# Optimization experiments

Hardware: AMD Instinct MI355X
Metric: run time of the kernel (lower is better)

Reference implementation:

```python
import jax, jax.numpy as jnp
from jax import lax
import numpy as np

B, L, V, E, D, T = 512, 200, 50000, 256, 256, 6
H = D // 2          # per-direction LSTM hidden
SLOPE = 0.01        # LeakyReLU negative slope
START, STOP = 4, 5  # tag_map['START'], tag_map['STOP']


def setup_inputs():
    key = jax.random.key(0)
    ks = jax.random.split(key, 18)
    w = lambda k, shape, scale=0.05: jax.random.normal(k, shape, jnp.float32) * scale
    trans = jax.random.normal(ks[17], (T, T), jnp.float32)
    trans = trans.at[:, START].set(-1000.0)
    trans = trans.at[STOP, :].set(-1000.0)
    return {
        "sentences": jax.random.randint(ks[0], (B, L), 0, V),
        "real_length": jnp.full((B,), L, dtype=jnp.int32),
        "emb": jax.random.normal(ks[1], (V, E), jnp.float32),
        "Wih_f": w(ks[2], (4 * H, E)), "Whh_f": w(ks[3], (4 * H, H)),
        "bih_f": w(ks[4], (4 * H,)),   "bhh_f": w(ks[5], (4 * H,)),
        "Wih_b": w(ks[6], (4 * H, E)), "Whh_b": w(ks[7], (4 * H, H)),
        "bih_b": w(ks[8], (4 * H,)),   "bhh_b": w(ks[9], (4 * H,)),
        "W1": w(ks[10], (D, D)), "b1": w(ks[11], (D,)),
        "W2": w(ks[12], (D, D)), "b2": w(ks[13], (D,)),
        "Wt": w(ks[14], (T, D)), "bt": w(ks[15], (T,)),
        "transitions": trans,
    }


def _leaky(x):
    return jnp.where(x >= 0, x, SLOPE * x)


def _lstm_dir(x, Wih, Whh, bih, bhh):
    # x: [B, L, E] -> hidden states [B, L, H]; PyTorch gate order i,f,g,o
    Bn = x.shape[0]
    Hn = Whh.shape[1]
    xg = jnp.einsum('ble,ge->blg', x, Wih) + bih + bhh  # [B, L, 4H]
    def step(carry, xt):
        h, c = carry
        g = xt + h @ Whh.T
        i, f, gg, o = jnp.split(g, 4, axis=-1)
        c = jax.nn.sigmoid(f) * c + jax.nn.sigmoid(i) * jnp.tanh(gg)
        h = jax.nn.sigmoid(o) * jnp.tanh(c)
        return (h, c), h
    init = (jnp.zeros((Bn, Hn), x.dtype), jnp.zeros((Bn, Hn), x.dtype))
    _, hs = lax.scan(step, init, jnp.swapaxes(xg, 0, 1))  # [L, B, H]
    return jnp.swapaxes(hs, 0, 1)


def _emissions(sentences, emb, Wih_f, Whh_f, bih_f, bhh_f, Wih_b, Whh_b, bih_b, bhh_b,
               W1, b1, W2, b2, Wt, bt):
    x = emb[sentences]                                   # [B, L, E]
    hf = _lstm_dir(x, Wih_f, Whh_f, bih_f, bhh_f)
    hb = _lstm_dir(x[:, ::-1], Wih_b, Whh_b, bih_b, bhh_b)[:, ::-1]
    h = jnp.concatenate([hf, hb], axis=-1)               # [B, L, D]
    h = _leaky(h @ W1.T + b1)
    h = _leaky(h @ W2.T + b2)
    return _leaky(h @ Wt.T + bt)                         # [B, L, T]


def _viterbi(logits, transitions):
    # logits: [L, T]; trellis recursion then backtrace
    def step(prev, obs):
        v = prev[:, None] + transitions                  # [T, T]
        tr = obs + jnp.max(v, axis=0)
        return tr, jnp.argmax(v, axis=0)
    last, bps = lax.scan(step, logits[0], logits[1:])    # bps: [L-1, T]
    score = jnp.max(last)
    last_tag = jnp.argmax(last)
    def back(tag, bp):
        new = bp[tag]
        return new, new
    _, prevs = lax.scan(back, last_tag, bps[::-1])
    path = jnp.concatenate([prevs[::-1], last_tag[None]])  # [L]
    return score, path


def reference(sentences, real_length, emb, Wih_f, Whh_f, bih_f, bhh_f,
              Wih_b, Whh_b, bih_b, bhh_b, W1, b1, W2, b2, Wt, bt, transitions):
    # real_length is full (=L) for every sample, so pack/pad is the identity,
    # matching the original forward's lengths=[i.size(-1)] behavior.
    logits = _emissions(sentences, emb, Wih_f, Whh_f, bih_f, bhh_f,
                        Wih_b, Whh_b, bih_b, bhh_b, W1, b1, W2, b2, Wt, bt)
    scores, paths = jax.vmap(_viterbi, in_axes=(0, None))(logits, transitions)
    return scores, paths
```

## Files before the change

### kernel.cpp

```cpp
#include <hip/hip_runtime.h>
#include <cmath>

#define B_   512
#define L_   200
#define V_   50000
#define E_   256
#define H_   128
#define G4H_ 512
#define D_   256
#define T_   6

__device__ __forceinline__ float sigmoidf_(float x) { return 1.0f / (1.0f + __expf(-x)); }
__device__ __forceinline__ float leakyf_(float x)   { return x >= 0.0f ? x : 0.01f * x; }

template<int CTRL>
__device__ __forceinline__ float dpp_add_(float x) {
    const int m = __builtin_amdgcn_mov_dpp(__float_as_int(x), CTRL, 0xF, 0xF, true);
    return x + __int_as_float(m);
}

#define XBM 128
#define XBN 128
#define XBK 8
#define XSTR 132

__global__ __launch_bounds__(256) void gemm_xg_chunk(
    const int* __restrict__ sent, const float* __restrict__ emb,
    const float* __restrict__ Wf, const float* __restrict__ Wb,
    const float* __restrict__ bihf, const float* __restrict__ bhhf,
    const float* __restrict__ bihb, const float* __restrict__ bhhb,
    float* __restrict__ xgc, int c0, int tc)
{
    __shared__ float As[2][XBK][XSTR];
    __shared__ float Bs[2][XBK][XSTR];
    __shared__ int   tok[XBM];

    const int bm  = blockIdx.x;
    const int bn  = blockIdx.y;
    const int tid = threadIdx.x;
    const int half = B_ * tc;
    const int dir  = (bm * XBM) >= half;

    if (tid < XBM) {
        const int vm  = bm * XBM + tid;
        const int rem = vm - dir * half;
        const int b   = rem / tc;
        const int ti  = rem - b * tc;
        const int s   = c0 + ti;
        const int t   = dir ? (L_ - 1 - s) : s;
        tok[tid] = sent[b * L_ + t];
    }
    __syncthreads();

    const int tx = tid & 15;
    const int ty = tid >> 4;
    const int n0 = bn * XBN;

    const float* W   = dir ? Wb   : Wf;
    const float* bih = dir ? bihb : bihf;
    const float* bhh = dir ? bhhb : bhhf;

    const int am = tid >> 1;
    const int ak = (tid & 1) * 4;

    const float* arow = emb + (size_t)tok[am] * E_ + ak;
    const float* brow = W + (size_t)(n0 + am) * E_ + ak;

    float acc[8][8];
#pragma unroll
    for (int i = 0; i < 8; ++i)
#pragma unroll
        for (int j = 0; j < 8; ++j) acc[i][j] = 0.0f;

    {
        const float4 a = *(const float4*)(arow);
        const float4 b = *(const float4*)(brow);
        As[0][ak + 0][am] = a.x; As[0][ak + 1][am] = a.y;
        As[0][ak + 2][am] = a.z; As[0][ak + 3][am] = a.w;
        Bs[0][ak + 0][am] = b.x; Bs[0][ak + 1][am] = b.y;
        Bs[0][ak + 2][am] = b.z; Bs[0][ak + 3][am] = b.w;
    }
    __syncthreads();

    const int NIT = E_ / XBK;
    for (int it = 0; it < NIT; ++it) {
        const int cur = it & 1;
        const int kn  = (it + 1) * XBK;
        float4 na, nb;
        if (kn < E_) {
            na = *(const float4*)(arow + kn);
            nb = *(const float4*)(brow + kn);
        }
#pragma unroll
        for (int k = 0; k < XBK; ++k) {
            float a[8], bb[8];
            *(float4*)a        = *(const float4*)&As[cur][k][ty * 4];
            *(float4*)(a + 4)  = *(const float4*)&As[cur][k][64 + ty * 4];
            *(float4*)(bb)     = *(const float4*)&Bs[cur][k][tx * 4];
            *(float4*)(bb + 4) = *(const float4*)&Bs[cur][k][64 + tx * 4];
#pragma unroll
            for (int i = 0; i < 8; ++i)
#pragma unroll
                for (int j = 0; j < 8; ++j) acc[i][j] += a[i] * bb[j];
        }
        if (kn < E_) {
            const int nxt = cur ^ 1;
            As[nxt][ak + 0][am] = na.x; As[nxt][ak + 1][am] = na.y;
            As[nxt][ak + 2][am] = na.z; As[nxt][ak + 3][am] = na.w;
            Bs[nxt][ak + 0][am] = nb.x; Bs[nxt][ak + 1][am] = nb.y;
            Bs[nxt][ak + 2][am] = nb.z; Bs[nxt][ak + 3][am] = nb.w;
        }
        __syncthreads();
    }

    const int nb0i = n0 + tx * 4;
    const int nb1i = n0 + 64 + tx * 4;
    float bias[8];
#pragma unroll
    for (int j = 0; j < 4; ++j) {
        bias[j]     = bih[nb0i + j] + bhh[nb0i + j];
        bias[4 + j] = bih[nb1i + j] + bhh[nb1i + j];
    }
#pragma unroll
    for (int i = 0; i < 8; ++i) {
        const int row = bm * XBM + ((i < 4) ? (ty * 4 + i) : (64 + ty * 4 + i - 4));
        float* dst = xgc + (size_t)row * G4H_;
        float4 v0, v1;
        v0.x = acc[i][0] + bias[0]; v0.y = acc[i][1] + bias[1];
        v0.z = acc[i][2] + bias[2]; v0.w = acc[i][3] + bias[3];
        v1.x = acc[i][4] + bias[4]; v1.y = acc[i][5] + bias[5];
        v1.z = acc[i][6] + bias[6]; v1.w = acc[i][7] + bias[7];
        *(float4*)(dst + nb0i) = v0;
        *(float4*)(dst + nb1i) = v1;
    }
}

__global__ __launch_bounds__(512, 2) void lstm_scan_chunk(
    const float* __restrict__ xgc,
    const float* __restrict__ Whh_f, const float* __restrict__ Whh_b,
    float* __restrict__ state, float* __restrict__ hcat, int c0, int tc)
{
    const int wg  = blockIdx.x;
    const int dir = wg >> 7;
    const int b0  = (wg & 127) * 4;
    const int tid = threadIdx.x;

    const int q  = tid & 3;
    const int g2 = tid >> 2;
    const int j_ = g2;
    const int s_ = q;

    const float* Whh = dir ? Whh_b : Whh_f;

    float w[4][32];
#pragma unroll
    for (int p = 0; p < 4; ++p) {
        const float* wr = Whh + (size_t)(g2 + 128 * p) * H_ + q * 32;
#pragma unroll
        for (int kk = 0; kk < 32; kk += 4) {
            const float4 v = *(const float4*)(wr + kk);
            w[p][kk] = v.x; w[p][kk + 1] = v.y; w[p][kk + 2] = v.z; w[p][kk + 3] = v.w;
        }
    }

    __shared__ float hbuf[4 * 132];
    __shared__ float gbuf[4 * 528];

    float c;
    if (c0 == 0) {
        hbuf[(j_ >> 5) * 132 + (j_ & 31) * 4 + s_] = 0.0f;
        c = 0.0f;
    } else {
        hbuf[(j_ >> 5) * 132 + (j_ & 31) * 4 + s_] =
            state[((size_t)(dir * B_ + b0 + s_) * 2 + 0) * H_ + j_];
        c = state[((size_t)(dir * B_ + b0 + s_) * 2 + 1) * H_ + j_];
    }

    const int t0    = dir ? (L_ - 1 - c0) : c0;
    const int hstep = dir ? -D_ : D_;
    const int grow  = g2 + 128 * q;

    const float* xp[4];
#pragma unroll
    for (int s = 0; s < 4; ++s)
        xp[s] = xgc + ((size_t)(dir * B_ + b0 + s) * tc) * G4H_ + grow;
    float* hp = hcat + ((size_t)(b0 + s_) * L_ + t0) * D_ + dir * H_ + j_;

    const float* hq = hbuf + q * 132;

    __syncthreads();

    for (int t = 0; t < tc; ++t) {
        float xv[4];
#pragma unroll
        for (int s = 0; s < 4; ++s) { xv[s] = xp[s][0]; xp[s] += G4H_; }

        float acc[4][4];
#pragma unroll
        for (int p = 0; p < 4; ++p)
#pragma unroll
            for (int s = 0; s < 4; ++s) acc[p][s] = 0.0f;

#pragma unroll
        for (int kk = 0; kk < 32; ++kk) {
            const float4 hv = *(const float4*)(hq + kk * 4);
#pragma unroll
            for (int p = 0; p < 4; ++p) {
                acc[p][0] += w[p][kk] * hv.x;
                acc[p][1] += w[p][kk] * hv.y;
                acc[p][2] += w[p][kk] * hv.z;
                acc[p][3] += w[p][kk] * hv.w;
            }
        }

#pragma unroll
        for (int p = 0; p < 4; ++p)
#pragma unroll
            for (int s = 0; s < 4; ++s) {
                float v = acc[p][s];
                v = dpp_add_<0xB1>(v);
                v = dpp_add_<0x4E>(v);
                acc[p][s] = v;
            }

        float o0 = acc[0][0], o1 = acc[0][1], o2 = acc[0][2], o3 = acc[0][3];
        if (q == 1) { o0 = acc[1][0]; o1 = acc[1][1]; o2 = acc[1][2]; o3 = acc[1][3]; }
        if (q == 2) { o0 = acc[2][0]; o1 = acc[2][1]; o2 = acc[2][2]; o3 = acc[2][3]; }
        if (q == 3) { o0 = acc[3][0]; o1 = acc[3][1]; o2 = acc[3][2]; o3 = acc[3][3]; }
        *(float4*)(gbuf + q * 528 + g2 * 4) =
            make_float4(o0 + xv[0], o1 + xv[1], o2 + xv[2], o3 + xv[3]);
        __syncthreads();

        {
            const float gi = gbuf[0 * 528 + j_ * 4 + s_];
            const float gf = gbuf[1 * 528 + j_ * 4 + s_];
            const float gg = gbuf[2 * 528 + j_ * 4 + s_];
            const float go = gbuf[3 * 528 + j_ * 4 + s_];
            c = sigmoidf_(gf) * c + sigmoidf_(gi) * tanhf(gg);
            const float hv = sigmoidf_(go) * tanhf(c);
            hbuf[(j_ >> 5) * 132 + (j_ & 31) * 4 + s_] = hv;
            hp[0] = hv;
            hp += hstep;
        }
        __syncthreads();
    }

    state[((size_t)(dir * B_ + b0 + s_) * 2 + 0) * H_ + j_] =
        hbuf[(j_ >> 5) * 132 + (j_ & 31) * 4 + s_];
    state[((size_t)(dir * B_ + b0 + s_) * 2 + 1) * H_ + j_] = c;
}

#define BM 64
#define BN 128
#define BK 16
#define ASTR 68
#define BSTR 132
#define S1T 68

__global__ __launch_bounds__(256) void fused_mlp(
    const float* __restrict__ hcat,
    const float* __restrict__ W1, const float* __restrict__ b1,
    const float* __restrict__ W2, const float* __restrict__ b2,
    const float* __restrict__ Wt, const float* __restrict__ bt,
    float* __restrict__ logits)
{
    __shared__ float As[BK][ASTR];
    __shared__ float Bs[BK][BSTR];
    __shared__ float h1T[BN][S1T];
    __shared__ float Wt_s[T_][D_ + 2];
    __shared__ float b1_s[D_], b2_s[D_], bt_s[T_];

    const int tid  = threadIdx.x;
    const int row0 = blockIdx.x * BM;

    for (int i = tid; i < T_ * D_; i += 256) Wt_s[i >> 8][i & 255] = Wt[i];
    b1_s[tid] = b1[tid];
    b2_s[tid] = b2[tid];
    if (tid < T_) bt_s[tid] = bt[tid];

    const int tx = tid & 15;
    const int ty = tid >> 4;
    const int lrow = tid >> 2;
    const int lk   = (tid & 3) * 4;

    const float* arow = hcat + (size_t)(row0 + lrow) * D_ + lk;

    float acc2[2][4][8];
#pragma unroll
    for (int q = 0; q < 2; ++q)
#pragma unroll
        for (int i = 0; i < 4; ++i)
#pragma unroll
            for (int j = 0; j < 8; ++j) acc2[q][i][j] = 0.0f;

    for (int n0t = 0; n0t < 2; ++n0t) {
        const int n0 = n0t * BN;

        float acc1[4][8];
#pragma unroll
        for (int i = 0; i < 4; ++i)
#pragma unroll
            for (int j = 0; j < 8; ++j) acc1[i][j] = 0.0f;

        for (int k0 = 0; k0 < D_; k0 += BK) {
            {
                const float4 v = *(const float4*)(arow + k0);
                As[lk + 0][lrow] = v.x; As[lk + 1][lrow] = v.y;
                As[lk + 2][lrow] = v.z; As[lk + 3][lrow] = v.w;
            }
#pragma unroll
            for (int p = 0; p < 2; ++p) {
                const int n = p * 64 + lrow;
                const float4 v = *(const float4*)(W1 + (size_t)(n0 + n) * D_ + k0 + lk);
                Bs[lk + 0][n] = v.x; Bs[lk + 1][n] = v.y;
                Bs[lk + 2][n] = v.z; Bs[lk + 3][n] = v.w;
            }
            __syncthreads();
#pragma unroll
            for (int k = 0; k < BK; ++k) {
                float a[4], bb[8];
                *(float4*)a        = *(const float4*)&As[k][ty * 4];
                *(float4*)(bb)     = *(const float4*)&Bs[k][tx * 4];
                *(float4*)(bb + 4) = *(const float4*)&Bs[k][64 + tx * 4];
#pragma unroll
                for (int i = 0; i < 4; ++i)
#pragma unroll
                    for (int j = 0; j < 8; ++j) acc1[i][j] += a[i] * bb[j];
            }
            __syncthreads();
        }

#pragma unroll
        for (int j = 0; j < 8; ++j) {
            const int nl = (j < 4) ? (tx * 4 + j) : (64 + tx * 4 + j - 4);
            const float bv = b1_s[n0 + nl];
            float4 v;
            v.x = leakyf_(acc1[0][j] + bv);
            v.y = leakyf_(acc1[1][j] + bv);
            v.z = leakyf_(acc1[2][j] + bv);
            v.w = leakyf_(acc1[3][j] + bv);
            *(float4*)&h1T[nl][ty * 4] = v;
        }
        __syncthreads();

#pragma unroll
        for (int n2t = 0; n2t < 2; ++n2t) {
            for (int kc = 0; kc < BN; kc += BK) {
#pragma unroll
                for (int p = 0; p < 2; ++p) {
                    const int n = p * 64 + lrow;
                    const float4 v = *(const float4*)(W2 + (size_t)(n2t * BN + n) * D_ + n0 + kc + lk);
                    Bs[lk + 0][n] = v.x; Bs[lk + 1][n] = v.y;
                    Bs[lk + 2][n] = v.z; Bs[lk + 3][n] = v.w;
                }
                __syncthreads();
#pragma unroll
                for (int k = 0; k < BK; ++k) {
                    float a[4], bb[8];
                    *(float4*)a        = *(const float4*)&h1T[kc + k][ty * 4];
                    *(float4*)(bb)     = *(const float4*)&Bs[k][tx * 4];
                    *(float4*)(bb + 4) = *(const float4*)&Bs[k][64 + tx * 4];
#pragma unroll
                    for (int i = 0; i < 4; ++i)
#pragma unroll
                        for (int j = 0; j < 8; ++j) acc2[n2t][i][j] += a[i] * bb[j];
                }
                __syncthreads();
            }
        }
    }

    float part[4][T_];
#pragma unroll
    for (int i = 0; i < 4; ++i)
#pragma unroll
        for (int jt = 0; jt < T_; ++jt) part[i][jt] = 0.0f;

#pragma unroll
    for (int q = 0; q < 2; ++q)
#pragma unroll
        for (int j = 0; j < 8; ++j) {
            const int n = q * BN + ((j < 4) ? (tx * 4 + j) : (64 + tx * 4 + j - 4));
            const float bv = b2_s[n];
            float h2v[4];
#pragma unroll
            for (int i = 0; i < 4; ++i) h2v[i] = leakyf_(acc2[q][i][j] + bv);
#pragma unroll
            for (int jt = 0; jt < T_; ++jt) {
                const float wv = Wt_s[jt][n];
#pragma unroll
                for (int i = 0; i < 4; ++i) part[i][jt] += h2v[i] * wv;
            }
        }

#pragma unroll
    for (int m = 1; m <= 8; m <<= 1)
#pragma unroll
        for (int i = 0; i < 4; ++i)
#pragma unroll
            for (int jt = 0; jt < T_; ++jt)
                part[i][jt] += __shfl_xor(part[i][jt], m, 16);

    if (tx == 0) {
#pragma unroll
        for (int i = 0; i < 4; ++i) {
            const int m = row0 + ty * 4 + i;
#pragma unroll
            for (int jt = 0; jt < T_; ++jt)
                logits[(size_t)m * T_ + jt] = leakyf_(part[i][jt] + bt_s[jt]);
        }
    }
}

__global__ __launch_bounds__(64) void viterbi_kernel(
    const float* __restrict__ logits, const float* __restrict__ trans,
    float* __restrict__ out)
{
    const int b = blockIdx.x;
    const int lane = threadIdx.x;

    __shared__ unsigned char bp[L_][8];
    __shared__ int path_s[L_];

    float tr[T_];
    if (lane < T_) {
#pragma unroll
        for (int i = 0; i < T_; ++i) tr[i] = trans[i * T_ + lane];
    }
    const float* lg = logits + (size_t)b * L_ * T_;
    float prev = (lane < T_) ? lg[lane] : -1e30f;

    for (int t = 1; t < L_; ++t) {
        float m = -1e30f; int arg = 0;
#pragma unroll
        for (int i = 0; i < T_; ++i) {
            const float v = __shfl(prev, i, 64) + tr[i];
            if (v > m) { m = v; arg = i; }
        }
        const float obs = (lane < T_) ? lg[t * T_ + lane] : 0.0f;
        prev = obs + m;
        if (lane < T_) bp[t][lane] = (unsigned char)arg;
    }
    __syncthreads();

    float best = __shfl(prev, 0, 64); int tag = 0;
#pragma unroll
    for (int jj = 1; jj < T_; ++jj) {
        const float v = __shfl(prev, jj, 64);
        if (v > best) { best = v; tag = jj; }
    }
    if (lane == 0) {
        out[b] = best;
        path_s[L_ - 1] = tag;
        for (int t = L_ - 1; t >= 1; --t) {
            tag = bp[t][tag];
            path_s[t - 1] = tag;
        }
    }
    __syncthreads();
    for (int i = lane; i < L_; i += 64)
        out[B_ + (size_t)b * L_ + i] = (float)path_s[i];
}

extern "C" void kernel_launch(void* const* d_in, const int* in_sizes, int n_in,
                              void* d_out, int out_size, void* d_ws, size_t ws_size,
                              hipStream_t stream)
{
    (void)in_sizes; (void)n_in; (void)out_size;

    const int*   sent  = (const int*)  d_in[0];
    const float* emb   = (const float*)d_in[2];
    const float* Wih_f = (const float*)d_in[3];
    const float* Whh_f = (const float*)d_in[4];
    const float* bih_f = (const float*)d_in[5];
    const float* bhh_f = (const float*)d_in[6];
    const float* Wih_b = (const float*)d_in[7];
    const float* Whh_b = (const float*)d_in[8];
    const float* bih_b = (const float*)d_in[9];
    const float* bhh_b = (const float*)d_in[10];
    const float* W1    = (const float*)d_in[11];
    const float* b1    = (const float*)d_in[12];
    const float* W2    = (const float*)d_in[13];
    const float* b2    = (const float*)d_in[14];
    const float* Wt    = (const float*)d_in[15];
    const float* bt    = (const float*)d_in[16];
    const float* trans = (const float*)d_in[17];

    float* ws = (float*)d_ws;
    const size_t HCAT_E = (size_t)B_ * L_ * D_;
    const size_t LG_E   = (size_t)B_ * L_ * T_;
    const size_t ST_E   = (size_t)2 * B_ * 2 * H_;
    float* hcat   = ws;
    float* logits = ws + HCAT_E;
    float* state  = logits + LG_E;
    float* xgc    = state + ST_E;

    const size_t base  = HCAT_E + LG_E + ST_E;
    const size_t per_t = (size_t)2 * B_ * G4H_;
    const size_t ws_f  = ws_size / sizeof(float);
    long long avail = (long long)ws_f - (long long)base;
    int Tc = (avail > 0) ? (int)(avail / (long long)per_t) : 0;
    if (Tc < 1)  Tc = 1;
    if (Tc > L_) Tc = L_;

    float* out = (float*)d_out;

    for (int c0 = 0; c0 < L_; c0 += Tc) {
        const int tc = (L_ - c0 < Tc) ? (L_ - c0) : Tc;
        gemm_xg_chunk<<<dim3(8 * tc, 4), 256, 0, stream>>>(
            sent, emb, Wih_f, Wih_b, bih_f, bhh_f, bih_b, bhh_b, xgc, c0, tc);
        lstm_scan_chunk<<<256, 512, 0, stream>>>(
            xgc, Whh_f, Whh_b, state, hcat, c0, tc);
    }
    fused_mlp<<<(B_ * L_) / BM, 256, 0, stream>>>(
        hcat, W1, b1, W2, b2, Wt, bt, logits);
    viterbi_kernel<<<B_, 64, 0, stream>>>(logits, trans, out);
}
```

Baseline: 1.804 ms.

## Widen input-gate GEMM tile to 128x256 and split MLP into two GEMM kernels

The input-projection GEMM now computes a 128x256 output tile per block (8x16 accumulators per thread), halving the grid's column dimension so each A tile (embedding gather) is reused across twice as many columns. The fused MLP is replaced, when workspace permits, by a layer-1 GEMM writing an intermediate h1 buffer into the xg workspace region, followed by a layer-2 GEMM with the tag projection fused in its epilogue through shuffle reductions. This aims to raise arithmetic intensity and GEMM efficiency, at the cost of higher register pressure and an extra round trip of the intermediate activations through global memory.

```diff
diff --git a/kernel.cpp b/kernel.cpp
--- a/kernel.cpp
+++ b/kernel.cpp
@@ -19,10 +19,10 @@
     return x + __int_as_float(m);
 }
 
-#define XBM 128
-#define XBN 128
-#define XBK 8
-#define XSTR 132
+#define XBM  128
+#define XBK  8
+#define XASTR 132
+#define XBSTR 264
 
 __global__ __launch_bounds__(256) void gemm_xg_chunk(
     const int* __restrict__ sent, const float* __restrict__ emb,
@@ -31,8 +31,8 @@
     const float* __restrict__ bihb, const float* __restrict__ bhhb,
     float* __restrict__ xgc, int c0, int tc)
 {
-    __shared__ float As[2][XBK][XSTR];
-    __shared__ float Bs[2][XBK][XSTR];
+    __shared__ float As[2][XBK][XASTR];
+    __shared__ float Bs[2][XBK][XBSTR];
     __shared__ int   tok[XBM];
 
     const int bm  = blockIdx.x;
@@ -54,7 +54,7 @@
 
     const int tx = tid & 15;
     const int ty = tid >> 4;
-    const int n0 = bn * XBN;
+    const int n0 = bn * 256;
 
     const float* W   = dir ? Wb   : Wf;
     const float* bih = dir ? bihb : bihf;
@@ -63,22 +63,26 @@
     const int am = tid >> 1;
     const int ak = (tid & 1) * 4;
 
-    const float* arow = emb + (size_t)tok[am] * E_ + ak;
-    const float* brow = W + (size_t)(n0 + am) * E_ + ak;
-
-    float acc[8][8];
+    const float* arow  = emb + (size_t)tok[am] * E_ + ak;
+    const float* brow0 = W + (size_t)(n0 + am) * E_ + ak;
+    const float* brow1 = W + (size_t)(n0 + 128 + am) * E_ + ak;
+
+    float acc[8][16];
 #pragma unroll
     for (int i = 0; i < 8; ++i)
 #pragma unroll
-        for (int j = 0; j < 8; ++j) acc[i][j] = 0.0f;
+        for (int j = 0; j < 16; ++j) acc[i][j] = 0.0f;
 
     {
-        const float4 a = *(const float4*)(arow);
-        const float4 b = *(const float4*)(brow);
-        As[0][ak + 0][am] = a.x; As[0][ak + 1][am] = a.y;
-        As[0][ak + 2][am] = a.z; As[0][ak + 3][am] = a.w;
-        Bs[0][ak + 0][am] = b.x; Bs[0][ak + 1][am] = b.y;
-        Bs[0][ak + 2][am] = b.z; Bs[0][ak + 3][am] = b.w;
+        const float4 a  = *(const float4*)(arow);
+        const float4 b0 = *(const float4*)(brow0);
+        const float4 b1 = *(const float4*)(brow1);
+        As[0][ak + 0][am] = a.x;  As[0][ak + 1][am] = a.y;
+        As[0][ak + 2][am] = a.z;  As[0][ak + 3][am] = a.w;
+        Bs[0][ak + 0][am] = b0.x; Bs[0][ak + 1][am] = b0.y;
+        Bs[0][ak + 2][am] = b0.z; Bs[0][ak + 3][am] = b0.w;
+        Bs[0][ak + 0][128 + am] = b1.x; Bs[0][ak + 1][128 + am] = b1.y;
+        Bs[0][ak + 2][128 + am] = b1.z; Bs[0][ak + 3][128 + am] = b1.w;
     }
     __syncthreads();
 
@@ -86,52 +90,58 @@
     for (int it = 0; it < NIT; ++it) {
         const int cur = it & 1;
         const int kn  = (it + 1) * XBK;
-        float4 na, nb;
+        float4 na, nb0, nb1;
         if (kn < E_) {
-            na = *(const float4*)(arow + kn);
-            nb = *(const float4*)(brow + kn);
+            na  = *(const float4*)(arow + kn);
+            nb0 = *(const float4*)(brow0 + kn);
+            nb1 = *(const float4*)(brow1 + kn);
         }
 #pragma unroll
         for (int k = 0; k < XBK; ++k) {
-            float a[8], bb[8];
-            *(float4*)a        = *(const float4*)&As[cur][k][ty * 4];
-            *(float4*)(a + 4)  = *(const float4*)&As[cur][k][64 + ty * 4];
-            *(float4*)(bb)     = *(const float4*)&Bs[cur][k][tx * 4];
-            *(float4*)(bb + 4) = *(const float4*)&Bs[cur][k][64 + tx * 4];
+            float a[8], bb[16];
+            *(float4*)a         = *(const float4*)&As[cur][k][ty * 4];
+            *(float4*)(a + 4)   = *(const float4*)&As[cur][k][64 + ty * 4];
+            *(float4*)(bb)      = *(const float4*)&Bs[cur][k][tx * 4];
+            *(float4*)(bb + 4)  = *(const float4*)&Bs[cur][k][64 + tx * 4];
+            *(float4*)(bb + 8)  = *(const float4*)&Bs[cur][k][128 + tx * 4];
+            *(float4*)(bb + 12) = *(const float4*)&Bs[cur][k][192 + tx * 4];
 #pragma unroll
             for (int i = 0; i < 8; ++i)
 #pragma unroll
-                for (int j = 0; j < 8; ++j) acc[i][j] += a[i] * bb[j];
+                for (int j = 0; j < 16; ++j) acc[i][j] += a[i] * bb[j];
         }
         if (kn < E_) {
             const int nxt = cur ^ 1;
-            As[nxt][ak + 0][am] = na.x; As[nxt][ak + 1][am] = na.y;
-            As[nxt][ak + 2][am] = na.z; As[nxt][ak + 3][am] = na.w;
-            Bs[nxt][ak + 0][am] = nb.x; Bs[nxt][ak + 1][am] = nb.y;
-            Bs[nxt][ak + 2][am] = nb.z; Bs[nxt][ak + 3][am] = nb.w;
+            As[nxt][ak + 0][am] = na.x;  As[nxt][ak + 1][am] = na.y;
+            As[nxt][ak + 2][am] = na.z;  As[nxt][ak + 3][am] = na.w;
+            Bs[nxt][ak + 0][am] = nb0.x; Bs[nxt][ak + 1][am] = nb0.y;
+            Bs[nxt][ak + 2][am] = nb0.z; Bs[nxt][ak + 3][am] = nb0.w;
+            Bs[nxt][ak + 0][128 + am] = nb1.x; Bs[nxt][ak + 1][128 + am] = nb1.y;
+            Bs[nxt][ak + 2][128 + am] = nb1.z; Bs[nxt][ak + 3][128 + am] = nb1.w;
         }
         __syncthreads();
     }
 
-    const int nb0i = n0 + tx * 4;
-    const int nb1i = n0 + 64 + tx * 4;
-    float bias[8];
-#pragma unroll
-    for (int j = 0; j < 4; ++j) {
-        bias[j]     = bih[nb0i + j] + bhh[nb0i + j];
-        bias[4 + j] = bih[nb1i + j] + bhh[nb1i + j];
+    float bias[16];
+#pragma unroll
+    for (int qd = 0; qd < 4; ++qd) {
+        const int cb = n0 + qd * 64 + tx * 4;
+#pragma unroll
+        for (int j = 0; j < 4; ++j) bias[qd * 4 + j] = bih[cb + j] + bhh[cb + j];
     }
 #pragma unroll
     for (int i = 0; i < 8; ++i) {
         const int row = bm * XBM + ((i < 4) ? (ty * 4 + i) : (64 + ty * 4 + i - 4));
         float* dst = xgc + (size_t)row * G4H_;
-        float4 v0, v1;
-        v0.x = acc[i][0] + bias[0]; v0.y = acc[i][1] + bias[1];
-        v0.z = acc[i][2] + bias[2]; v0.w = acc[i][3] + bias[3];
-        v1.x = acc[i][4] + bias[4]; v1.y = acc[i][5] + bias[5];
-        v1.z = acc[i][6] + bias[6]; v1.w = acc[i][7] + bias[7];
-        *(float4*)(dst + nb0i) = v0;
-        *(float4*)(dst + nb1i) = v1;
+#pragma unroll
+        for (int qd = 0; qd < 4; ++qd) {
+            float4 v;
+            v.x = acc[i][qd * 4 + 0] + bias[qd * 4 + 0];
+            v.y = acc[i][qd * 4 + 1] + bias[qd * 4 + 1];
+            v.z = acc[i][qd * 4 + 2] + bias[qd * 4 + 2];
+            v.w = acc[i][qd * 4 + 3] + bias[qd * 4 + 3];
+            *(float4*)(dst + n0 + qd * 64 + tx * 4) = v;
+        }
     }
 }
 
@@ -248,6 +258,227 @@
     state[((size_t)(dir * B_ + b0 + s_) * 2 + 0) * H_ + j_] =
         hbuf[(j_ >> 5) * 132 + (j_ & 31) * 4 + s_];
     state[((size_t)(dir * B_ + b0 + s_) * 2 + 1) * H_ + j_] = c;
+}
+
+__global__ __launch_bounds__(256) void mlp1_gemm(
+    const float* __restrict__ hcat,
+    const float* __restrict__ W1, const float* __restrict__ b1,
+    float* __restrict__ h1)
+{
+    __shared__ float As[2][XBK][XASTR];
+    __shared__ float Bs[2][XBK][XBSTR];
+
+    const int bm  = blockIdx.x;
+    const int tid = threadIdx.x;
+    const int tx = tid & 15;
+    const int ty = tid >> 4;
+
+    const int am = tid >> 1;
+    const int ak = (tid & 1) * 4;
+
+    const float* arow  = hcat + (size_t)(bm * XBM + am) * D_ + ak;
+    const float* brow0 = W1 + (size_t)am * D_ + ak;
+    const float* brow1 = W1 + (size_t)(128 + am) * D_ + ak;
+
+    float acc[8][16];
+#pragma unroll
+    for (int i = 0; i < 8; ++i)
+#pragma unroll
+        for (int j = 0; j < 16; ++j) acc[i][j] = 0.0f;
+
+    {
+        const float4 a  = *(const float4*)(arow);
+        const float4 b0 = *(const float4*)(brow0);
+        const float4 b1v = *(const float4*)(brow1);
+        As[0][ak + 0][am] = a.x;  As[0][ak + 1][am] = a.y;
+        As[0][ak + 2][am] = a.z;  As[0][ak + 3][am] = a.w;
+        Bs[0][ak + 0][am] = b0.x; Bs[0][ak + 1][am] = b0.y;
+        Bs[0][ak + 2][am] = b0.z; Bs[0][ak + 3][am] = b0.w;
+        Bs[0][ak + 0][128 + am] = b1v.x; Bs[0][ak + 1][128 + am] = b1v.y;
+        Bs[0][ak + 2][128 + am] = b1v.z; Bs[0][ak + 3][128 + am] = b1v.w;
+    }
+    __syncthreads();
+
+    const int NIT = D_ / XBK;
+    for (int it = 0; it < NIT; ++it) {
+        const int cur = it & 1;
+        const int kn  = (it + 1) * XBK;
+        float4 na, nb0, nb1;
+        if (kn < D_) {
+            na  = *(const float4*)(arow + kn);
+            nb0 = *(const float4*)(brow0 + kn);
+            nb1 = *(const float4*)(brow1 + kn);
+        }
+#pragma unroll
+        for (int k = 0; k < XBK; ++k) {
+            float a[8], bb[16];
+            *(float4*)a         = *(const float4*)&As[cur][k][ty * 4];
+            *(float4*)(a + 4)   = *(const float4*)&As[cur][k][64 + ty * 4];
+            *(float4*)(bb)      = *(const float4*)&Bs[cur][k][tx * 4];
+            *(float4*)(bb + 4)  = *(const float4*)&Bs[cur][k][64 + tx * 4];
+            *(float4*)(bb + 8)  = *(const float4*)&Bs[cur][k][128 + tx * 4];
+            *(float4*)(bb + 12) = *(const float4*)&Bs[cur][k][192 + tx * 4];
+#pragma unroll
+            for (int i = 0; i < 8; ++i)
+#pragma unroll
+                for (int j = 0; j < 16; ++j) acc[i][j] += a[i] * bb[j];
+        }
+        if (kn < D_) {
+            const int nxt = cur ^ 1;
+            As[nxt][ak + 0][am] = na.x;  As[nxt][ak + 1][am] = na.y;
+            As[nxt][ak + 2][am] = na.z;  As[nxt][ak + 3][am] = na.w;
+            Bs[nxt][ak + 0][am] = nb0.x; Bs[nxt][ak + 1][am] = nb0.y;
+            Bs[nxt][ak + 2][am] = nb0.z; Bs[nxt][ak + 3][am] = nb0.w;
+            Bs[nxt][ak + 0][128 + am] = nb1.x; Bs[nxt][ak + 1][128 + am] = nb1.y;
+            Bs[nxt][ak + 2][128 + am] = nb1.z; Bs[nxt][ak + 3][128 + am] = nb1.w;
+        }
+        __syncthreads();
+    }
+
+    float bias[16];
+#pragma unroll
+    for (int qd = 0; qd < 4; ++qd) {
+        const int cb = qd * 64 + tx * 4;
+#pragma unroll
+        for (int j = 0; j < 4; ++j) bias[qd * 4 + j] = b1[cb + j];
+    }
+#pragma unroll
+    for (int i = 0; i < 8; ++i) {
+        const int row = bm * XBM + ((i < 4) ? (ty * 4 + i) : (64 + ty * 4 + i - 4));
+        float* dst = h1 + (size_t)row * D_;
+#pragma unroll
+        for (int qd = 0; qd < 4; ++qd) {
+            float4 v;
+            v.x = leakyf_(acc[i][qd * 4 + 0] + bias[qd * 4 + 0]);
+            v.y = leakyf_(acc[i][qd * 4 + 1] + bias[qd * 4 + 1]);
+            v.z = leakyf_(acc[i][qd * 4 + 2] + bias[qd * 4 + 2]);
+            v.w = leakyf_(acc[i][qd * 4 + 3] + bias[qd * 4 + 3]);
+            *(float4*)(dst + qd * 64 + tx * 4) = v;
+        }
+    }
+}
+
+__global__ __launch_bounds__(256) void mlp2tag(
+    const float* __restrict__ h1,
+    const float* __restrict__ W2, const float* __restrict__ b2,
+    const float* __restrict__ Wt, const float* __restrict__ bt,
+    float* __restrict__ logits)
+{
+    __shared__ float As[2][XBK][XASTR];
+    __shared__ float Bs[2][XBK][XBSTR];
+    __shared__ float Wt_s[T_][D_ + 2];
+    __shared__ float b2_s[D_];
+    __shared__ float bt_s[T_];
+
+    const int bm  = blockIdx.x;
+    const int tid = threadIdx.x;
+    const int tx = tid & 15;
+    const int ty = tid >> 4;
+
+    for (int i = tid; i < T_ * D_; i += 256) Wt_s[i >> 8][i & 255] = Wt[i];
+    b2_s[tid] = b2[tid];
+    if (tid < T_) bt_s[tid] = bt[tid];
+
+    const int am = tid >> 1;
+    const int ak = (tid & 1) * 4;
+
+    const float* arow  = h1 + (size_t)(bm * XBM + am) * D_ + ak;
+    const float* brow0 = W2 + (size_t)am * D_ + ak;
+    const float* brow1 = W2 + (size_t)(128 + am) * D_ + ak;
+
+    float acc[8][16];
+#pragma unroll
+    for (int i = 0; i < 8; ++i)
+#pragma unroll
+        for (int j = 0; j < 16; ++j) acc[i][j] = 0.0f;
+
+    {
+        const float4 a  = *(const float4*)(arow);
+        const float4 b0 = *(const float4*)(brow0);
+        const float4 b1v = *(const float4*)(brow1);
+        As[0][ak + 0][am] = a.x;  As[0][ak + 1][am] = a.y;
+        As[0][ak + 2][am] = a.z;  As[0][ak + 3][am] = a.w;
+        Bs[0][ak + 0][am] = b0.x; Bs[0][ak + 1][am] = b0.y;
+        Bs[0][ak + 2][am] = b0.z; Bs[0][ak + 3][am] = b0.w;
+        Bs[0][ak + 0][128 + am] = b1v.x; Bs[0][ak + 1][128 + am] = b1v.y;
+        Bs[0][ak + 2][128 + am] = b1v.z; Bs[0][ak + 3][128 + am] = b1v.w;
+    }
+    __syncthreads();
+
+    const int NIT = D_ / XBK;
+    for (int it = 0; it < NIT; ++it) {
+        const int cur = it & 1;
+        const int kn  = (it + 1) * XBK;
+        float4 na, nb0, nb1;
+        if (kn < D_) {
+            na  = *(const float4*)(arow + kn);
+            nb0 = *(const float4*)(brow0 + kn);
+            nb1 = *(const float4*)(brow1 + kn);
+        }
+#pragma unroll
+        for (int k = 0; k < XBK; ++k) {
+            float a[8], bb[16];
+            *(float4*)a         = *(const float4*)&As[cur][k][ty * 4];
+            *(float4*)(a + 4)   = *(const float4*)&As[cur][k][64 + ty * 4];
+            *(float4*)(bb)      = *(const float4*)&Bs[cur][k][tx * 4];
+            *(float4*)(bb + 4)  = *(const float4*)&Bs[cur][k][64 + tx * 4];
+            *(float4*)(bb + 8)  = *(const float4*)&Bs[cur][k][128 + tx * 4];
+            *(float4*)(bb + 12) = *(const float4*)&Bs[cur][k][192 + tx * 4];
+#pragma unroll
+            for (int i = 0; i < 8; ++i)
+#pragma unroll
+                for (int j = 0; j < 16; ++j) acc[i][j] += a[i] * bb[j];
+        }
+        if (kn < D_) {
+            const int nxt = cur ^ 1;
+            As[nxt][ak + 0][am] = na.x;  As[nxt][ak + 1][am] = na.y;
+            As[nxt][ak + 2][am] = na.z;  As[nxt][ak + 3][am] = na.w;
+            Bs[nxt][ak + 0][am] = nb0.x; Bs[nxt][ak + 1][am] = nb0.y;
+            Bs[nxt][ak + 2][am] = nb0.z; Bs[nxt][ak + 3][am] = nb0.w;
+            Bs[nxt][ak + 0][128 + am] = nb1.x; Bs[nxt][ak + 1][128 + am] = nb1.y;
+            Bs[nxt][ak + 2][128 + am] = nb1.z; Bs[nxt][ak + 3][128 + am] = nb1.w;
+        }
+        __syncthreads();
+    }
+
+    float part[8][T_];
+#pragma unroll
+    for (int i = 0; i < 8; ++i)
+#pragma unroll
+        for (int jt = 0; jt < T_; ++jt) part[i][jt] = 0.0f;
+
+#pragma unroll
+    for (int j = 0; j < 16; ++j) {
+        const int n = (j >> 2) * 64 + tx * 4 + (j & 3);
+        const float bv = b2_s[n];
+        float h2v[8];
+#pragma unroll
+        for (int i = 0; i < 8; ++i) h2v[i] = leakyf_(acc[i][j] + bv);
+#pragma unroll
+        for (int jt = 0; jt < T_; ++jt) {
+            const float wv = Wt_s[jt][n];
+#pragma unroll
+            for (int i = 0; i < 8; ++i) part[i][jt] += h2v[i] * wv;
+        }
+    }
+
+#pragma unroll
+    for (int m = 1; m <= 8; m <<= 1)
+#pragma unroll
+        for (int i = 0; i < 8; ++i)
+#pragma unroll
+            for (int jt = 0; jt < T_; ++jt)
+                part[i][jt] += __shfl_xor(part[i][jt], m, 16);
+
+    if (tx == 0) {
+#pragma unroll
+        for (int i = 0; i < 8; ++i) {
+            const int row = bm * XBM + ((i < 4) ? (ty * 4 + i) : (64 + ty * 4 + i - 4));
+#pragma unroll
+            for (int jt = 0; jt < T_; ++jt)
+                logits[(size_t)row * T_ + jt] = leakyf_(part[i][jt] + bt_s[jt]);
+        }
+    }
 }
 
 #define BM 64
@@ -490,6 +721,7 @@
     const size_t HCAT_E = (size_t)B_ * L_ * D_;
     const size_t LG_E   = (size_t)B_ * L_ * T_;
     const size_t ST_E   = (size_t)2 * B_ * 2 * H_;
+    const size_t H1_E   = HCAT_E;
     float* hcat   = ws;
     float* logits = ws + HCAT_E;
     float* state  = logits + LG_E;
@@ -507,12 +739,19 @@
 
     for (int c0 = 0; c0 < L_; c0 += Tc) {
         const int tc = (L_ - c0 < Tc) ? (L_ - c0) : Tc;
-        gemm_xg_chunk<<<dim3(8 * tc, 4), 256, 0, stream>>>(
+        gemm_xg_chunk<<<dim3(8 * tc, 2), 256, 0, stream>>>(
             sent, emb, Wih_f, Wih_b, bih_f, bhh_f, bih_b, bhh_b, xgc, c0, tc);
         lstm_scan_chunk<<<256, 512, 0, stream>>>(
             xgc, Whh_f, Whh_b, state, hcat, c0, tc);
     }
-    fused_mlp<<<(B_ * L_) / BM, 256, 0, stream>>>(
-        hcat, W1, b1, W2, b2, Wt, bt, logits);
+
+    if (avail >= (long long)H1_E) {
+        float* h1 = xgc;
+        mlp1_gemm<<<(B_ * L_) / XBM, 256, 0, stream>>>(hcat, W1, b1, h1);
+        mlp2tag<<<(B_ * L_) / XBM, 256, 0, stream>>>(h1, W2, b2, Wt, bt, logits);
+    } else {
+        fused_mlp<<<(B_ * L_) / BM, 256, 0, stream>>>(
+            hcat, W1, b1, W2, b2, Wt, bt, logits);
+    }
     viterbi_kernel<<<B_, 64, 0, stream>>>(logits, trans, out);
 }
```

Result: slower. 2.283 ms (+26.6%).

## Keep LSTM gates in registers and double-buffer hidden state to drop a barrier

Applied to the files above, without the earlier changes.

Each thread selects its own sample's four gate values from the quad-reduced accumulators instead of writing them to a shared gate buffer and reading them back. The hidden state uses two shared buffers alternated by step parity, so each timestep needs one barrier instead of two. This removes the shared-memory round trip and one synchronisation per step in the sequential recurrence. The cost is a small amount of extra shared memory for the second hidden buffer.

```diff
diff --git a/kernel.cpp b/kernel.cpp
--- a/kernel.cpp
+++ b/kernel.cpp
@@ -147,8 +147,6 @@
 
     const int q  = tid & 3;
     const int g2 = tid >> 2;
-    const int j_ = g2;
-    const int s_ = q;
 
     const float* Whh = dir ? Whh_b : Whh_f;
 
@@ -163,37 +161,34 @@
         }
     }
 
-    __shared__ float hbuf[4 * 132];
-    __shared__ float gbuf[4 * 528];
-
-    float c;
+    __shared__ float hbuf[2][4 * 132];
+
+    float c, hval;
     if (c0 == 0) {
-        hbuf[(j_ >> 5) * 132 + (j_ & 31) * 4 + s_] = 0.0f;
-        c = 0.0f;
+        hval = 0.0f;
+        c    = 0.0f;
     } else {
-        hbuf[(j_ >> 5) * 132 + (j_ & 31) * 4 + s_] =
-            state[((size_t)(dir * B_ + b0 + s_) * 2 + 0) * H_ + j_];
-        c = state[((size_t)(dir * B_ + b0 + s_) * 2 + 1) * H_ + j_];
-    }
+        hval = state[((size_t)(dir * B_ + b0 + q) * 2 + 0) * H_ + g2];
+        c    = state[((size_t)(dir * B_ + b0 + q) * 2 + 1) * H_ + g2];
+    }
+    hbuf[0][(g2 >> 5) * 132 + (g2 & 31) * 4 + q] = hval;
 
     const int t0    = dir ? (L_ - 1 - c0) : c0;
     const int hstep = dir ? -D_ : D_;
-    const int grow  = g2 + 128 * q;
-
-    const float* xp[4];
-#pragma unroll
-    for (int s = 0; s < 4; ++s)
-        xp[s] = xgc + ((size_t)(dir * B_ + b0 + s) * tc) * G4H_ + grow;
-    float* hp = hcat + ((size_t)(b0 + s_) * L_ + t0) * D_ + dir * H_ + j_;
-
-    const float* hq = hbuf + q * 132;
+
+    const float* xq = xgc + ((size_t)(dir * B_ + b0 + q) * tc) * G4H_ + g2;
+    float* hp = hcat + ((size_t)(b0 + q) * L_ + t0) * D_ + dir * H_ + g2;
 
     __syncthreads();
 
     for (int t = 0; t < tc; ++t) {
-        float xv[4];
-#pragma unroll
-        for (int s = 0; s < 4; ++s) { xv[s] = xp[s][0]; xp[s] += G4H_; }
+        const int par = t & 1;
+        const float* hq = &hbuf[par][q * 132];
+
+        float xg[4];
+#pragma unroll
+        for (int p = 0; p < 4; ++p) xg[p] = xq[128 * p];
+        xq += G4H_;
 
         float acc[4][4];
 #pragma unroll
@@ -223,31 +218,23 @@
                 acc[p][s] = v;
             }
 
-        float o0 = acc[0][0], o1 = acc[0][1], o2 = acc[0][2], o3 = acc[0][3];
-        if (q == 1) { o0 = acc[1][0]; o1 = acc[1][1]; o2 = acc[1][2]; o3 = acc[1][3]; }
-        if (q == 2) { o0 = acc[2][0]; o1 = acc[2][1]; o2 = acc[2][2]; o3 = acc[2][3]; }
-        if (q == 3) { o0 = acc[3][0]; o1 = acc[3][1]; o2 = acc[3][2]; o3 = acc[3][3]; }
-        *(float4*)(gbuf + q * 528 + g2 * 4) =
-            make_float4(o0 + xv[0], o1 + xv[1], o2 + xv[2], o3 + xv[3]);
+        float gi = acc[0][0], gf = acc[1][0], gg = acc[2][0], go = acc[3][0];
+        if (q == 1) { gi = acc[0][1]; gf = acc[1][1]; gg = acc[2][1]; go = acc[3][1]; }
+        if (q == 2) { gi = acc[0][2]; gf = acc[1][2]; gg = acc[2][2]; go = acc[3][2]; }
+        if (q == 3) { gi = acc[0][3]; gf = acc[1][3]; gg = acc[2][3]; go = acc[3][3]; }
+        gi += xg[0]; gf += xg[1]; gg += xg[2]; go += xg[3];
+
+        c    = sigmoidf_(gf) * c + sigmoidf_(gi) * tanhf(gg);
+        hval = sigmoidf_(go) * tanhf(c);
+
+        hbuf[par ^ 1][(g2 >> 5) * 132 + (g2 & 31) * 4 + q] = hval;
+        hp[0] = hval;
+        hp += hstep;
         __syncthreads();
-
-        {
-            const float gi = gbuf[0 * 528 + j_ * 4 + s_];
-            const float gf = gbuf[1 * 528 + j_ * 4 + s_];
-            const float gg = gbuf[2 * 528 + j_ * 4 + s_];
-            const float go = gbuf[3 * 528 + j_ * 4 + s_];
-            c = sigmoidf_(gf) * c + sigmoidf_(gi) * tanhf(gg);
-            const float hv = sigmoidf_(go) * tanhf(c);
-            hbuf[(j_ >> 5) * 132 + (j_ & 31) * 4 + s_] = hv;
-            hp[0] = hv;
-            hp += hstep;
-        }
-        __syncthreads();
-    }
-
-    state[((size_t)(dir * B_ + b0 + s_) * 2 + 0) * H_ + j_] =
-        hbuf[(j_ >> 5) * 132 + (j_ & 31) * 4 + s_];
-    state[((size_t)(dir * B_ + b0 + s_) * 2 + 1) * H_ + j_] = c;
+    }
+
+    state[((size_t)(dir * B_ + b0 + q) * 2 + 0) * H_ + g2] = hval;
+    state[((size_t)(dir * B_ + b0 + q) * 2 + 1) * H_ + g2] = c;
 }
 
 #define BM 64
```

Measured after the change: 1.816 ms, median of 3. Within noise of the previous version (+0.7%).
